# Performance work log

Measured on AMD Instinct MI355X. Metric: run time of the kernel, lower is better.

## Reference

```python
import jax, jax.numpy as jnp
import numpy as np

B, S, D = 4, 1024, 1024
NH, DH = 16, 64
DI = 4096
EPS = 1e-5


def layer_norm(x, g, b):
    mu = jnp.mean(x, axis=-1, keepdims=True)
    var = jnp.mean(jnp.square(x - mu), axis=-1, keepdims=True)
    return (x - mu) * jax.lax.rsqrt(var + EPS) * g + b


def rel_shift(x):
    # x: [B, n, q, r] -> Transformer-XL relative shift + lower-tri mask
    b, n, q, r = x.shape
    zp = jnp.zeros((b, n, q, 1), x.dtype)
    xp = jnp.concatenate([zp, x], axis=3).reshape(b, n, r + 1, q)
    x = xp[:, :, 1:, :].reshape(b, n, q, r)
    tril = jnp.tril(jnp.ones((q, r), x.dtype), r - q)
    return x * tril[None, None]


def setup_inputs() -> dict:
    key = jax.random.key(0)
    ks = jax.random.split(key, 16)
    sc = 0.02
    return {
        "w": jax.random.normal(ks[0], (B, S, D), jnp.float32),
        "r": jax.random.normal(ks[1], (B, S, D), jnp.float32),
        "w_bias": jax.random.normal(ks[2], (NH, 1, DH), jnp.float32) * sc,
        "r_bias": jax.random.normal(ks[3], (NH, 1, DH), jnp.float32) * sc,
        "Wq": jax.random.normal(ks[4], (D, NH * DH), jnp.float32) * sc,
        "Wk": jax.random.normal(ks[5], (D, NH * DH), jnp.float32) * sc,
        "Wv": jax.random.normal(ks[6], (D, NH * DH), jnp.float32) * sc,
        "Wr": jax.random.normal(ks[7], (D, NH * DH), jnp.float32) * sc,
        "Wo": jax.random.normal(ks[8], (NH * DH, D), jnp.float32) * sc,
        "ln1_g": jnp.ones((D,), jnp.float32),
        "ln1_b": jnp.zeros((D,), jnp.float32),
        "W1": jax.random.normal(ks[9], (D, DI), jnp.float32) * sc,
        "b1": jnp.zeros((DI,), jnp.float32),
        "W2": jax.random.normal(ks[10], (DI, D), jnp.float32) * sc,
        "b2": jnp.zeros((D,), jnp.float32),
        "ln2_g": jnp.ones((D,), jnp.float32),
        "ln2_b": jnp.zeros((D,), jnp.float32),
    }


def reference(w, r, w_bias, r_bias, Wq, Wk, Wv, Wr, Wo,
              ln1_g, ln1_b, W1, b1, W2, b2, ln2_g, ln2_b):
    b, q_len, _ = w.shape
    k_len = q_len
    scale = 1.0 / (DH ** 0.5)

    def heads(x):
        return x.reshape(b, -1, NH, DH).transpose(0, 2, 1, 3)  # [B, n, S, d]

    q = heads(w @ Wq)
    k = heads(w @ Wk)
    v = heads(w @ Wv)
    rr = heads(r @ Wr)

    ac = jnp.einsum('bnid,bnjd->bnij', q + w_bias[None], k)
    bd = rel_shift(jnp.einsum('bnid,bnjd->bnij', q + r_bias[None], rr))
    attn_score = (ac + bd) * scale

    mask = jnp.triu(jnp.ones((q_len, k_len), bool), 1)
    attn_score = jnp.where(mask[None, None], jnp.float32(-1e9), attn_score)
    attn_prob = jax.nn.softmax(attn_score, axis=-1)

    attn_vec = jnp.einsum('bnij,bnjd->bnid', attn_prob, v)
    attn_vec = attn_vec.transpose(0, 2, 1, 3).reshape(b, q_len, NH * DH)
    attn_out = attn_vec @ Wo

    x = layer_norm(w + attn_out, ln1_g, ln1_b)
    ff = jax.nn.relu(x @ W1 + b1) @ W2 + b2
    return layer_norm(x + ff, ln2_g, ln2_b)
```

## Files before the change

### kernel.cpp

```cpp
#include <hip/hip_runtime.h>
#include <hip/hip_bf16.h>

using bf16 = __hip_bfloat16;
typedef __attribute__((ext_vector_type(8))) short bf16x8;
typedef __attribute__((ext_vector_type(4))) float f32x4;

static constexpr int TB  = 4;
static constexpr int TS  = 1024;
static constexpr int TD  = 1024;
static constexpr int TNH = 16;
static constexpr int TDH = 64;
static constexpr int TDI = 4096;

__device__ __forceinline__ void gll16(const bf16* g, bf16* l)
{
    __builtin_amdgcn_global_load_lds(
        (const __attribute__((address_space(1))) void*)g,
        (__attribute__((address_space(3))) void*)l, 16, 0, 0);
}

__global__ __launch_bounds__(256) void zero_out_k(float* __restrict__ out, long n)
{
    long i = (long)blockIdx.x * 256 + threadIdx.x;
    if (i < n) out[i] = 0.0f;
}

__global__ __launch_bounds__(256) void convert2_f2b(const float* __restrict__ a,
                                                    const float* __restrict__ b,
                                                    bf16* __restrict__ oa,
                                                    bf16* __restrict__ ob, long n)
{
    const float* src = blockIdx.y ? b : a;
    bf16* dst = blockIdx.y ? ob : oa;
    long i = ((long)blockIdx.x * 256 + threadIdx.x) * 8;
    if (i >= n) return;
    float4 f0 = *(const float4*)(src + i);
    float4 f1 = *(const float4*)(src + i + 4);
    bf16 t[8] = {__float2bfloat16(f0.x), __float2bfloat16(f0.y),
                 __float2bfloat16(f0.z), __float2bfloat16(f0.w),
                 __float2bfloat16(f1.x), __float2bfloat16(f1.y),
                 __float2bfloat16(f1.z), __float2bfloat16(f1.w)};
    *(bf16x8*)(dst + i) = *(bf16x8*)t;
}

__global__ __launch_bounds__(256) void transpose_f2b(const float* __restrict__ in,
                                                     bf16* __restrict__ out,
                                                     int R, int C)
{
    __shared__ float tile[32][33];
    int c0 = blockIdx.x * 32, r0 = blockIdx.y * 32;
    int tx = threadIdx.x & 31, ty = threadIdx.x >> 5;
#pragma unroll
    for (int dy = 0; dy < 32; dy += 8)
        tile[ty + dy][tx] = in[(long)(r0 + ty + dy) * C + (c0 + tx)];
    __syncthreads();
#pragma unroll
    for (int dy = 0; dy < 32; dy += 8)
        out[(long)(c0 + ty + dy) * R + (r0 + tx)] = __float2bfloat16(tile[tx][ty + dy]);
}

__global__ __launch_bounds__(256) void transpose5_f2b(const float* __restrict__ p0,
                                                      const float* __restrict__ p1,
                                                      const float* __restrict__ p2,
                                                      const float* __restrict__ p3,
                                                      const float* __restrict__ p4,
                                                      bf16* __restrict__ dstBase)
{
    __shared__ float tile[32][33];
    const int D = TD;
    int z = blockIdx.z;
    const float* in = (z == 0) ? p0 : (z == 1) ? p1 : (z == 2) ? p2 : (z == 3) ? p3 : p4;
    bf16* out = dstBase + (long)z * D * D;
    int c0 = blockIdx.x * 32, r0 = blockIdx.y * 32;
    int tx = threadIdx.x & 31, ty = threadIdx.x >> 5;
#pragma unroll
    for (int dy = 0; dy < 32; dy += 8)
        tile[ty + dy][tx] = in[(long)(r0 + ty + dy) * D + (c0 + tx)];
    __syncthreads();
#pragma unroll
    for (int dy = 0; dy < 32; dy += 8)
        out[(long)(c0 + ty + dy) * D + (r0 + tx)] = __float2bfloat16(tile[tx][ty + dy]);
}

__global__ __launch_bounds__(256) void transpose_v(const bf16* __restrict__ V,
                                                   bf16* __restrict__ Vpk)
{
    __shared__ bf16 tile[32][33];
    int bn = blockIdx.z;
    int b = bn >> 4, n = bn & 15;
    const bf16* src = V + ((long)b * TS) * (TNH * TDH) + n * TDH;
    bf16* dst = Vpk + (long)bn * 65536;
    int s0 = blockIdx.x * 32, d0 = blockIdx.y * 32;
    int tx = threadIdx.x & 31, ty = threadIdx.x >> 5;
#pragma unroll
    for (int dy = 0; dy < 32; dy += 8)
        tile[ty + dy][tx] = src[(long)(s0 + ty + dy) * (TNH * TDH) + (d0 + tx)];
    __syncthreads();
#pragma unroll
    for (int dy = 0; dy < 32; dy += 8) {
        int d = d0 + ty + dy, s = s0 + tx;
        dst[((d >> 4) * 128 + (s >> 3)) * 128 + (d & 15) * 8 + (s & 7)] =
            tile[tx][ty + dy];
    }
}


__device__ __forceinline__ void stage_half(const bf16* __restrict__ X, long ldx,
                                           long rbase, long kcol,
                                           bf16* lds, int srow)
{
    gll16(X + (rbase + srow) * ldx + kcol, lds);
    gll16(X + (rbase + 128 + srow) * ldx + kcol, lds + 4096);
}

template<int MODE>
__global__ __launch_bounds__(512, 2) void gemm256_k(
    const bf16* __restrict__ A, long lda,
    const bf16* __restrict__ Bt, long ldb,
    bf16* __restrict__ O0, bf16* __restrict__ O1,
    bf16* __restrict__ O2, bf16* __restrict__ O3,
    float* __restrict__ F0, float* __restrict__ F1,
    float* __restrict__ F2, float* __restrict__ F3,
    const float* __restrict__ bias,
    int Kz, int GY, long ldc)
{
    __shared__ bf16 LDSbf[65536];

    const int z = blockIdx.y;
    const long kb = (long)z * Kz;
    const int NT = Kz >> 6;
    const int NI = NT >> 1;

    const int nwg = gridDim.x;
    const int orig = blockIdx.x;
    const int q = nwg >> 3, r = nwg & 7;
    const int xcd = orig & 7, idx = orig >> 3;
    const int wgid = (xcd < r ? xcd * (q + 1) : r * (q + 1) + (xcd - r) * q) + idx;

    int tx, ty;
    if (MODE == 1) {
        if (wgid < 192) { ty = wgid & 15; tx = wgid >> 4; }
        else { int w2 = wgid - 192; ty = 16 + (w2 & 15); tx = 12 + (w2 >> 4); }
    } else {
        ty = wgid % GY; tx = wgid / GY;
    }
    const long row0 = (long)ty * 256;
    const int col0 = tx * 256;

    const int tid = threadIdx.x;
    const int lane = tid & 63;
    const int wave = tid >> 6;
    const int wm2 = wave >> 2;
    const int wn4 = wave & 3;
    const int l15 = lane & 15;
    const int lq  = lane >> 4;

    const int slot = ((l15 & 1) << 2) | (lq ^ ((l15 >> 1) & 3));
    const int rdA = (wm2 * 64 + (l15 >> 1)) * 64 + slot * 8;
    const int rdB = 16384 + (wn4 * 32 + (l15 >> 1)) * 64 + slot * 8;

    const int srow  = wave * 16 + ((lane >> 3) << 1) + ((lane >> 2) & 1);
    const int scol8 = ((lane & 3) ^ ((lane >> 3) & 3)) * 8;

    f32x4 acc[8][4] = {};
    bf16x8 af[8], bb[4];

#define SA(t, db, kh) stage_half(A, lda, row0, kb + (long)(t) * 64 + (kh) * 32 + scol8, \
                                 LDSbf + (db) * 32768 + (kh) * 8192 + wave * 512, srow)
#define SB(t, db, kh) stage_half(Bt, ldb, (long)col0, kb + (long)(t) * 64 + (kh) * 32 + scol8, \
                                 LDSbf + (db) * 32768 + 16384 + (kh) * 8192 + wave * 512, srow)
#define RD_A(bp, kh) do {                                                              \
    _Pragma("unroll")                                                                  \
    for (int i_ = 0; i_ < 8; ++i_)                                                     \
        af[i_] = *(const bf16x8*)(LDSbf + (bp) * 32768 + (kh) * 8192 + rdA + i_ * 512);\
    } while (0)
#define RD_B(bp, kh, jh) do {                                                          \
    bb[(jh)*2]   = *(const bf16x8*)(LDSbf + (bp)*32768 + (kh)*8192 + rdB + ((jh)*2)*512);   \
    bb[(jh)*2+1] = *(const bf16x8*)(LDSbf + (bp)*32768 + (kh)*8192 + rdB + ((jh)*2+1)*512); \
    } while (0)
#define MM(jh) do {                                                                    \
    __builtin_amdgcn_s_setprio(1);                                                     \
    _Pragma("unroll")                                                                  \
    for (int i_ = 0; i_ < 8; ++i_) {                                                   \
        acc[i_][(jh)*2]   = __builtin_amdgcn_mfma_f32_16x16x32_bf16(af[i_], bb[(jh)*2],   acc[i_][(jh)*2],   0, 0, 0); \
        acc[i_][(jh)*2+1] = __builtin_amdgcn_mfma_f32_16x16x32_bf16(af[i_], bb[(jh)*2+1], acc[i_][(jh)*2+1], 0, 0, 0); \
    }                                                                                  \
    __builtin_amdgcn_s_setprio(0);                                                     \
    } while (0)
#define BAR       __builtin_amdgcn_s_barrier()
#define WLGKM0    do { asm volatile("s_waitcnt lgkmcnt(0)" ::: "memory");              \
                       __builtin_amdgcn_sched_barrier(0); } while (0)
#define WVM6      asm volatile("s_waitcnt vmcnt(6)" ::: "memory")

    SA(0, 0, 0); SB(0, 0, 0); SA(0, 0, 1); SB(0, 0, 1); SA(1, 1, 0);
    WVM6; BAR;

    for (int it = 0; it < NI; ++it) {
        const int T  = 2 * it;
        const int t1 = T + 1;
        const int t2 = (T + 2 < NT) ? T + 2 : NT - 1;
        const int t3 = (T + 3 < NT) ? T + 3 : NT - 1;

        RD_A(0, 0); RD_B(0, 0, 0); SB(t1, 1, 0);
        BAR; WLGKM0; MM(0); BAR;
        RD_B(0, 0, 1); SA(t1, 1, 1);
        BAR; WLGKM0; MM(1); WVM6; BAR;
        RD_A(0, 1); RD_B(0, 1, 0); SB(t1, 1, 1);
        BAR; WLGKM0; MM(0); BAR;
        RD_B(0, 1, 1); SA(t2, 0, 0);
        BAR; WLGKM0; MM(1); WVM6; BAR;
        RD_A(1, 0); RD_B(1, 0, 0); SB(t2, 0, 0);
        BAR; WLGKM0; MM(0); BAR;
        RD_B(1, 0, 1); SA(t2, 0, 1);
        BAR; WLGKM0; MM(1); WVM6; BAR;
        RD_A(1, 1); RD_B(1, 1, 0); SB(t2, 0, 1);
        BAR; WLGKM0; MM(0); BAR;
        RD_B(1, 1, 1); SA(t3, 1, 0);
        BAR; WLGKM0; MM(1); WVM6; BAR;
    }
    asm volatile("s_waitcnt vmcnt(0)" ::: "memory");

#undef SA
#undef SB
#undef RD_A
#undef RD_B
#undef MM
#undef BAR
#undef WLGKM0
#undef WVM6

    if (MODE == 0) {
        float* F = (z == 0) ? F0 : (z == 1) ? F1 : (z == 2) ? F2 : F3;
#pragma unroll
        for (int i = 0; i < 8; ++i) {
            long rb = (row0 + wm2 * 128 + i * 16 + lq * 4) * ldc;
#pragma unroll
            for (int j = 0; j < 4; ++j) {
                int nc = col0 + wn4 * 64 + j * 16 + l15;
#pragma unroll
                for (int rg = 0; rg < 4; ++rg)
                    F[rb + (long)rg * ldc + nc] = acc[i][j][rg];
            }
        }
    } else if (MODE == 1) {
        const int sel = tx >> 2;
        bf16* O = (sel == 0) ? O0 : (sel == 1) ? O1 : (sel == 2) ? O2 : O3;
        const int coladj = sel << 10;
        const long rowadj = (sel == 3) ? 4096 : 0;
#pragma unroll
        for (int i = 0; i < 8; ++i) {
            long mrow0 = row0 - rowadj + wm2 * 128 + i * 16 + lq * 4;
#pragma unroll
            for (int j = 0; j < 4; ++j) {
                int nc = col0 - coladj + wn4 * 64 + j * 16 + l15;
#pragma unroll
                for (int rg = 0; rg < 4; ++rg) {
                    float v = acc[i][j][rg];
                    if (sel == 0) v += bias[nc];
                    long mrow = mrow0 + rg;
                    if (sel == 2) {
                        O[mrow * 1024 + nc] = __float2bfloat16(v);
                    } else {
                        long b_ = mrow >> 10;
                        int s  = (int)mrow & 1023;
                        int n_ = nc >> 6, d = nc & 63;
                        long pidx = ((b_ * 16 + n_) << 16)
                                  + ((s >> 4) * 8 + (d >> 3)) * 128
                                  + (s & 15) * 8 + (d & 7);
                        O[pidx] = __float2bfloat16(v);
                    }
                }
            }
        }
    } else {
#pragma unroll
        for (int i = 0; i < 8; ++i) {
            long rb = (row0 + wm2 * 128 + i * 16 + lq * 4) * ldc;
#pragma unroll
            for (int j = 0; j < 4; ++j) {
                int nc = col0 + wn4 * 64 + j * 16 + l15;
#pragma unroll
                for (int rg = 0; rg < 4; ++rg) {
                    float v = acc[i][j][rg] + bias[nc];
                    v = fmaxf(v, 0.0f);
                    O0[rb + (long)rg * ldc + nc] = __float2bfloat16(v);
                }
            }
        }
    }
}

__global__ __launch_bounds__(64, 2) void flash_attn(
    const bf16* __restrict__ Qpk, const bf16* __restrict__ Kpk,
    const bf16* __restrict__ RRpk, const bf16* __restrict__ Vpk,
    const float* __restrict__ wbias, const float* __restrict__ rbias,
    bf16* __restrict__ Oa)
{
    const int S = TS, D = TD;
    __shared__ bf16 scr[32 * 161];

    const int orig = blockIdx.x;
    const int xcd = orig & 7, idx = orig >> 3;
    const int bn = xcd * 8 + (idx & 7);
    const int rem = idx >> 3;
    const int it = 7 - (rem >> 2);
    const int dw = (rem & 3) * 32;
    const int i0 = it * 128;
    const int b = bn >> 4, n = bn & 15;

    const int lane = threadIdx.x;
    const int l15 = lane & 15, lq = lane >> 4;

    const bf16* Qb = Qpk  + (long)bn * 65536;
    const bf16* Kb = Kpk  + (long)bn * 65536;
    const bf16* Rb = RRpk + (long)bn * 65536;
    const bf16* Vb = Vpk  + (long)bn * 65536;

    bf16x8 afw[2][2], afr[2][2];
#pragma unroll
    for (int m = 0; m < 2; ++m)
#pragma unroll
        for (int ks = 0; ks < 2; ++ks) {
            afw[m][ks] = *(const bf16x8*)(
                Qb + ((((i0 + dw) >> 4) + m) * 8 + ks * 4 + lq) * 128 + l15 * 8);
            bf16 tmp[8];
#pragma unroll
            for (int jj = 0; jj < 8; ++jj) {
                int di_ = n * 64 + ks * 32 + lq * 8 + jj;
                float f = __bfloat162float(((const bf16*)&afw[m][ks])[jj])
                          + rbias[di_] - wbias[di_];
                tmp[jj] = __float2bfloat16(f);
            }
            afr[m][ks] = *(bf16x8*)tmp;
        }

    float mst[2][4], lst[2][4];
    f32x4 Oacc[2][4] = {};
#pragma unroll
    for (int m = 0; m < 2; ++m)
#pragma unroll
        for (int rg = 0; rg < 4; ++rg) { mst[m][rg] = -1e30f; lst[m][rg] = 0.0f; }

    const int cofsg = 992 - i0 - dw;

    for (int jt = 0; jt <= it; ++jt) {
        const int j0 = jt * 128;
        const int rbt = (j0 + cofsg) >> 4;

#pragma unroll
        for (int g = 0; g < 2; ++g) {
            f32x4 bdl[2][5] = {};
#pragma unroll
            for (int ks = 0; ks < 2; ++ks) {
                bf16x8 bfr[5];
#pragma unroll
                for (int f = 0; f < 5; ++f) {
                    int t = rbt + g * 5 + f;
                    if (t > 63) t = 63;
                    bfr[f] = *(const bf16x8*)(Rb + (t * 8 + ks * 4 + lq) * 128 + l15 * 8);
                }
#pragma unroll
                for (int m = 0; m < 2; ++m)
#pragma unroll
                    for (int f = 0; f < 5; ++f)
                        bdl[m][f] = __builtin_amdgcn_mfma_f32_16x16x32_bf16(
                            afr[m][ks], bfr[f], bdl[m][f], 0, 0, 0);
            }
#pragma unroll
            for (int m = 0; m < 2; ++m)
#pragma unroll
                for (int f = 0; f < 5; ++f)
#pragma unroll
                    for (int rg = 0; rg < 4; ++rg) {
                        int ldi = lq * 4 + rg + 16 * m;
                        scr[ldi * 161 + (g * 5 + f) * 16 + l15] =
                            __float2bfloat16(bdl[m][f][rg]);
                    }
        }

        f32x4 ac[2][8] = {};
#pragma unroll
        for (int ks = 0; ks < 2; ++ks) {
            bf16x8 bk[8];
#pragma unroll
            for (int f = 0; f < 8; ++f)
                bk[f] = *(const bf16x8*)(
                    Kb + (((j0 >> 4) + f) * 8 + ks * 4 + lq) * 128 + l15 * 8);
#pragma unroll
            for (int m = 0; m < 2; ++m)
#pragma unroll
                for (int f = 0; f < 8; ++f)
                    ac[m][f] = __builtin_amdgcn_mfma_f32_16x16x32_bf16(
                        afw[m][ks], bk[f], ac[m][f], 0, 0, 0);
        }

        const bool diag = (jt == it);
#pragma unroll
        for (int m = 0; m < 2; ++m)
#pragma unroll
            for (int nf = 0; nf < 8; ++nf)
#pragma unroll
                for (int rg = 0; rg < 4; ++rg) {
                    int ldi = lq * 4 + rg + 16 * m;
                    int col = nf * 16 + l15;
                    float bdv = __bfloat162float(scr[ldi * 161 + (col + 31 - ldi)]);
                    float s = (ac[m][nf][rg] + bdv) * 0.125f;
                    if (diag && (col > dw + ldi)) s = -1e30f;
                    ac[m][nf][rg] = s;
                }

        float alpha[2][4];
#pragma unroll
        for (int m = 0; m < 2; ++m)
#pragma unroll
            for (int rg = 0; rg < 4; ++rg) {
                float v = -1e30f;
#pragma unroll
                for (int nf = 0; nf < 8; ++nf) v = fmaxf(v, ac[m][nf][rg]);
                for (int o = 8; o; o >>= 1) v = fmaxf(v, __shfl_xor(v, o));
                float mn = fmaxf(mst[m][rg], v);
                alpha[m][rg] = __expf(mst[m][rg] - mn);
                mst[m][rg] = mn;
            }
#pragma unroll
        for (int m = 0; m < 2; ++m)
#pragma unroll
            for (int nf = 0; nf < 8; ++nf)
#pragma unroll
                for (int rg = 0; rg < 4; ++rg)
                    ac[m][nf][rg] = __expf(ac[m][nf][rg] - mst[m][rg]);
#pragma unroll
        for (int m = 0; m < 2; ++m)
#pragma unroll
            for (int rg = 0; rg < 4; ++rg) {
                float sv = 0.0f;
#pragma unroll
                for (int nf = 0; nf < 8; ++nf) sv += ac[m][nf][rg];
                for (int o = 8; o; o >>= 1) sv += __shfl_xor(sv, o);
                lst[m][rg] = lst[m][rg] * alpha[m][rg] + sv;
            }
#pragma unroll
        for (int m = 0; m < 2; ++m)
#pragma unroll
            for (int nf = 0; nf < 4; ++nf)
#pragma unroll
                for (int rg = 0; rg < 4; ++rg)
                    Oacc[m][nf][rg] *= alpha[m][rg];

#pragma unroll
        for (int m = 0; m < 2; ++m)
#pragma unroll
            for (int nf = 0; nf < 8; ++nf)
#pragma unroll
                for (int rg = 0; rg < 4; ++rg) {
                    int ldi = lq * 4 + rg + 16 * m;
                    scr[ldi * 136 + nf * 16 + l15] = __float2bfloat16(ac[m][nf][rg]);
                }
#pragma unroll
        for (int ks2 = 0; ks2 < 4; ++ks2) {
            bf16x8 pa[2];
#pragma unroll
            for (int m = 0; m < 2; ++m)
                pa[m] = *(const bf16x8*)(&scr[(16 * m + l15) * 136 + ks2 * 32 + lq * 8]);
            bf16x8 vb[4];
#pragma unroll
            for (int nf = 0; nf < 4; ++nf)
                vb[nf] = *(const bf16x8*)(
                    Vb + (nf * 128 + (j0 >> 3) + ks2 * 4 + lq) * 128 + l15 * 8);
#pragma unroll
            for (int m = 0; m < 2; ++m)
#pragma unroll
                for (int nf = 0; nf < 4; ++nf)
                    Oacc[m][nf] = __builtin_amdgcn_mfma_f32_16x16x32_bf16(
                        pa[m], vb[nf], Oacc[m][nf], 0, 0, 0);
        }
    }

#pragma unroll
    for (int m = 0; m < 2; ++m)
#pragma unroll
        for (int rg = 0; rg < 4; ++rg) {
            float inv = 1.0f / lst[m][rg];
#pragma unroll
            for (int nf = 0; nf < 4; ++nf) {
                int row = i0 + dw + lq * 4 + rg + 16 * m;
                int col = nf * 16 + l15;
                Oa[((long)(b * S + row)) * D + n * 64 + col] =
                    __float2bfloat16(Oacc[m][nf][rg] * inv);
            }
        }
}

__global__ __launch_bounds__(256) void layernorm_f(const float* __restrict__ A0,
                                                   const float* __restrict__ A1,
                                                   const float* __restrict__ A2,
                                                   const float* __restrict__ A3,
                                                   const float* __restrict__ bias,
                                                   const float* __restrict__ residf,
                                                   const bf16* __restrict__ residb,
                                                   const float* __restrict__ g,
                                                   const float* __restrict__ beta,
                                                   float* __restrict__ Yf,
                                                   bf16* __restrict__ Yb)
{
    const int D = TD;
    long row = blockIdx.x;
    int tid = threadIdx.x;
    int wave = tid >> 6;

    float v[4], s = 0.0f;
#pragma unroll
    for (int it = 0; it < 4; ++it) {
        int c = tid + it * 256;
        float x = A0[row * D + c] + A1[row * D + c] + A2[row * D + c] + A3[row * D + c];
        if (bias)   x += bias[c];
        if (residf) x += residf[row * D + c];
        if (residb) x += __bfloat162float(residb[row * D + c]);
        v[it] = x; s += x;
    }
    for (int off = 32; off; off >>= 1) s += __shfl_xor(s, off);
    __shared__ float sm[8];
    if ((tid & 63) == 0) sm[wave] = s;
    __syncthreads();
    float mean = (sm[0] + sm[1] + sm[2] + sm[3]) * (1.0f / D);

    float var = 0.0f;
#pragma unroll
    for (int it = 0; it < 4; ++it) { float d = v[it] - mean; var += d * d; }
    for (int off = 32; off; off >>= 1) var += __shfl_xor(var, off);
    if ((tid & 63) == 0) sm[4 + wave] = var;
    __syncthreads();
    var = (sm[4] + sm[5] + sm[6] + sm[7]) * (1.0f / D);
    float rinv = rsqrtf(var + 1e-5f);

#pragma unroll
    for (int it = 0; it < 4; ++it) {
        int c = tid + it * 256;
        float o = (v[it] - mean) * rinv * g[c] + beta[c];
        if (Yf) Yf[row * D + c] = o;
        if (Yb) Yb[row * D + c] = __float2bfloat16(o);
    }
}

extern "C" void kernel_launch(void* const* d_in, const int* in_sizes, int n_in,
                              void* d_out, int out_size, void* d_ws, size_t ws_size,
                              hipStream_t stream)
{
    const float* w      = (const float*)d_in[0];
    const float* r      = (const float*)d_in[1];
    const float* w_bias = (const float*)d_in[2];
    const float* r_bias = (const float*)d_in[3];
    const float* Wq     = (const float*)d_in[4];
    const float* Wk     = (const float*)d_in[5];
    const float* Wv     = (const float*)d_in[6];
    const float* Wr     = (const float*)d_in[7];
    const float* Wo     = (const float*)d_in[8];
    const float* ln1_g  = (const float*)d_in[9];
    const float* ln1_b  = (const float*)d_in[10];
    const float* W1     = (const float*)d_in[11];
    const float* b1     = (const float*)d_in[12];
    const float* W2     = (const float*)d_in[13];
    const float* b2     = (const float*)d_in[14];
    const float* ln2_g  = (const float*)d_in[15];
    const float* ln2_b  = (const float*)d_in[16];
    float* out = (float*)d_out;

    const int  B = TB, S = TS, D = TD, NH = TNH, DH = TDH, DI = TDI;
    const long MS = (long)B * S;
    const long ND = (long)MS * D;

    char* base = (char*)d_ws;
    size_t off = 0;
    auto alloc = [&](size_t bytes) -> void* {
        void* p = base + off;
        off += (bytes + 255) & ~(size_t)255;
        return p;
    };
    bf16* wqT  = (bf16*)alloc(2UL * D * D);
    bf16* wkT  = (bf16*)alloc(2UL * D * D);
    bf16* wvT  = (bf16*)alloc(2UL * D * D);
    bf16* wrT  = (bf16*)alloc(2UL * D * D);
    bf16* woT  = (bf16*)alloc(2UL * D * D);
    bf16* w1T  = (bf16*)alloc(2UL * D * DI);
    bf16* w2T  = (bf16*)alloc(2UL * DI * D);
    bf16* bufA = (bf16*)alloc(2UL * ND);
    bf16* bufB = (bf16*)alloc(2UL * ND);
    bf16* Qpk  = (bf16*)alloc(2UL * ND);
    bf16* Kpk  = (bf16*)alloc(2UL * ND);
    bf16* RRpk = (bf16*)alloc(2UL * ND);
    bf16* Vpk  = (bf16*)alloc(2UL * ND);
    bf16* R0   = (bf16*)alloc(2UL * MS * DI);
    size_t need = off;
    (void)in_sizes; (void)n_in; (void)out_size;

    if (ws_size < need) {
        zero_out_k<<<dim3((unsigned)((ND + 255) / 256)), 256, 0, stream>>>(out, ND);
        return;
    }

    bf16* w_bf = bufA;  bf16* attn_vec = bufA;
    bf16* r_bf = bufB;  bf16* x_bf     = bufB;
    bf16* Vb   = R0;    bf16* h        = R0;
    float* Pf  = (float*)Qpk;

    convert2_f2b<<<dim3((unsigned)(ND / (8 * 256)), 2), 256, 0, stream>>>(
        w, r, w_bf, r_bf, ND);
    transpose5_f2b<<<dim3(D / 32, D / 32, 5), 256, 0, stream>>>(
        Wq, Wk, Wv, Wr, Wo, wqT);
    transpose_f2b<<<dim3(DI / 32, D / 32), 256, 0, stream>>>(W1, w1T, D, DI);
    transpose_f2b<<<dim3(D / 32, DI / 32), 256, 0, stream>>>(W2, w2T, DI, D);

    gemm256_k<1><<<dim3(256, 1), 512, 0, stream>>>(
        w_bf, D, wqT, D, Qpk, Kpk, Vb, RRpk,
        nullptr, nullptr, nullptr, nullptr, w_bias, D, 16, D);
    transpose_v<<<dim3(S / 32, DH / 32, B * NH), 256, 0, stream>>>(Vb, Vpk);

    flash_attn<<<dim3(2048), 64, 0, stream>>>(Qpk, Kpk, RRpk, Vpk, w_bias, r_bias,
                                              attn_vec);

    gemm256_k<0><<<dim3(64, 4), 512, 0, stream>>>(
        attn_vec, D, woT, D, nullptr, nullptr, nullptr, nullptr,
        Pf, Pf + ND, Pf + 2 * ND, Pf + 3 * ND, nullptr, D / 4, 16, D);
    layernorm_f<<<dim3((unsigned)MS), 256, 0, stream>>>(
        Pf, Pf + ND, Pf + 2 * ND, Pf + 3 * ND, nullptr, w, nullptr,
        ln1_g, ln1_b, nullptr, x_bf);

    gemm256_k<2><<<dim3(256, 1), 512, 0, stream>>>(
        x_bf, D, w1T, D, h, nullptr, nullptr, nullptr,
        nullptr, nullptr, nullptr, nullptr, b1, D, 16, DI);

    gemm256_k<0><<<dim3(64, 4), 512, 0, stream>>>(
        h, DI, w2T, DI, nullptr, nullptr, nullptr, nullptr,
        Pf, Pf + ND, (float*)wqT, out, nullptr, DI / 4, 16, D);
    layernorm_f<<<dim3((unsigned)MS), 256, 0, stream>>>(
        Pf, Pf + ND, (float*)wqT, out, b2, nullptr, x_bf,
        ln2_g, ln2_b, out, nullptr);
}
```

Baseline: 411.1 us.

## Replace split-K output GEMMs with 128-tile GEMMs, fuse V packing, shrink attention tiles

The Wo and W2 projections no longer use a 4-way split-K 256-tile GEMM that wrote four fp32 partials for layernorm to sum. They now use a new 128x128-tile GEMM that adds bias and residual in its epilogue and writes a single fp32 result, which a simpler layernorm reads. The QKV GEMM writes V directly in the packed layout the attention kernel needs, so the separate transpose kernel is removed. Flash attention processes 16 query rows per wave instead of 32, with twice as many blocks and higher occupancy, at the cost of more K/V reloads across waves.

```diff
diff --git a/kernel.cpp b/kernel.cpp
--- a/kernel.cpp
+++ b/kernel.cpp
@@ -82,28 +82,6 @@
         out[(long)(c0 + ty + dy) * D + (r0 + tx)] = __float2bfloat16(tile[tx][ty + dy]);
 }
 
-__global__ __launch_bounds__(256) void transpose_v(const bf16* __restrict__ V,
-                                                   bf16* __restrict__ Vpk)
-{
-    __shared__ bf16 tile[32][33];
-    int bn = blockIdx.z;
-    int b = bn >> 4, n = bn & 15;
-    const bf16* src = V + ((long)b * TS) * (TNH * TDH) + n * TDH;
-    bf16* dst = Vpk + (long)bn * 65536;
-    int s0 = blockIdx.x * 32, d0 = blockIdx.y * 32;
-    int tx = threadIdx.x & 31, ty = threadIdx.x >> 5;
-#pragma unroll
-    for (int dy = 0; dy < 32; dy += 8)
-        tile[ty + dy][tx] = src[(long)(s0 + ty + dy) * (TNH * TDH) + (d0 + tx)];
-    __syncthreads();
-#pragma unroll
-    for (int dy = 0; dy < 32; dy += 8) {
-        int d = d0 + ty + dy, s = s0 + tx;
-        dst[((d >> 4) * 128 + (s >> 3)) * 128 + (d & 15) * 8 + (s & 7)] =
-            tile[tx][ty + dy];
-    }
-}
-
 
 __device__ __forceinline__ void stage_half(const bf16* __restrict__ X, long ldx,
                                            long rbase, long kcol,
@@ -119,16 +97,12 @@
     const bf16* __restrict__ Bt, long ldb,
     bf16* __restrict__ O0, bf16* __restrict__ O1,
     bf16* __restrict__ O2, bf16* __restrict__ O3,
-    float* __restrict__ F0, float* __restrict__ F1,
-    float* __restrict__ F2, float* __restrict__ F3,
     const float* __restrict__ bias,
-    int Kz, int GY, long ldc)
+    int K, int GY, long ldc)
 {
     __shared__ bf16 LDSbf[65536];
 
-    const int z = blockIdx.y;
-    const long kb = (long)z * Kz;
-    const int NT = Kz >> 6;
+    const int NT = K >> 6;
     const int NI = NT >> 1;
 
     const int nwg = gridDim.x;
@@ -165,9 +139,9 @@
     f32x4 acc[8][4] = {};
     bf16x8 af[8], bb[4];
 
-#define SA(t, db, kh) stage_half(A, lda, row0, kb + (long)(t) * 64 + (kh) * 32 + scol8, \
+#define SA(t, db, kh) stage_half(A, lda, row0, (long)(t) * 64 + (kh) * 32 + scol8, \
                                  LDSbf + (db) * 32768 + (kh) * 8192 + wave * 512, srow)
-#define SB(t, db, kh) stage_half(Bt, ldb, (long)col0, kb + (long)(t) * 64 + (kh) * 32 + scol8, \
+#define SB(t, db, kh) stage_half(Bt, ldb, (long)col0, (long)(t) * 64 + (kh) * 32 + scol8, \
                                  LDSbf + (db) * 32768 + 16384 + (kh) * 8192 + wave * 512, srow)
 #define RD_A(bp, kh) do {                                                              \
     _Pragma("unroll")                                                                  \
@@ -229,20 +203,7 @@
 #undef WLGKM0
 #undef WVM6
 
-    if (MODE == 0) {
-        float* F = (z == 0) ? F0 : (z == 1) ? F1 : (z == 2) ? F2 : F3;
-#pragma unroll
-        for (int i = 0; i < 8; ++i) {
-            long rb = (row0 + wm2 * 128 + i * 16 + lq * 4) * ldc;
-#pragma unroll
-            for (int j = 0; j < 4; ++j) {
-                int nc = col0 + wn4 * 64 + j * 16 + l15;
-#pragma unroll
-                for (int rg = 0; rg < 4; ++rg)
-                    F[rb + (long)rg * ldc + nc] = acc[i][j][rg];
-            }
-        }
-    } else if (MODE == 1) {
+    if (MODE == 1) {
         const int sel = tx >> 2;
         bf16* O = (sel == 0) ? O0 : (sel == 1) ? O1 : (sel == 2) ? O2 : O3;
         const int coladj = sel << 10;
@@ -258,17 +219,18 @@
                     float v = acc[i][j][rg];
                     if (sel == 0) v += bias[nc];
                     long mrow = mrow0 + rg;
+                    long b_ = mrow >> 10;
+                    int s  = (int)mrow & 1023;
+                    int n_ = nc >> 6, d = nc & 63;
+                    long pidx;
                     if (sel == 2) {
-                        O[mrow * 1024 + nc] = __float2bfloat16(v);
+                        pidx = ((b_ * 16 + n_) << 16)
+                             + ((d >> 4) * 128 + (s >> 3)) * 128 + (d & 15) * 8 + (s & 7);
                     } else {
-                        long b_ = mrow >> 10;
-                        int s  = (int)mrow & 1023;
-                        int n_ = nc >> 6, d = nc & 63;
-                        long pidx = ((b_ * 16 + n_) << 16)
-                                  + ((s >> 4) * 8 + (d >> 3)) * 128
-                                  + (s & 15) * 8 + (d & 7);
-                        O[pidx] = __float2bfloat16(v);
+                        pidx = ((b_ * 16 + n_) << 16)
+                             + ((s >> 4) * 8 + (d >> 3)) * 128 + (s & 15) * 8 + (d & 7);
                     }
+                    O[pidx] = __float2bfloat16(v);
                 }
             }
         }
@@ -290,22 +252,137 @@
     }
 }
 
-__global__ __launch_bounds__(64, 2) void flash_attn(
+template<int MODE>
+__global__ __launch_bounds__(512, 2) void gemm128_k(
+    const bf16* __restrict__ A, long lda,
+    const bf16* __restrict__ Bt, long ldb,
+    float* __restrict__ Zf,
+    const float* __restrict__ residf, const bf16* __restrict__ residb,
+    const float* __restrict__ bias,
+    int K, int GY, long ldc)
+{
+    __shared__ bf16 LDSbf[32768];
+
+    const int NT = K >> 6;
+    const int NI = NT >> 1;
+
+    const int nwg = gridDim.x;
+    const int orig = blockIdx.x;
+    const int q = nwg >> 3, r = nwg & 7;
+    const int xcd = orig & 7, idx = orig >> 3;
+    const int wgid = (xcd < r ? xcd * (q + 1) : r * (q + 1) + (xcd - r) * q) + idx;
+
+    const int ty = wgid % GY, tx = wgid / GY;
+    const long row0 = (long)ty * 128;
+    const long col0 = (long)tx * 128;
+
+    const int tid = threadIdx.x;
+    const int lane = tid & 63;
+    const int wave = tid >> 6;
+    const int wm2 = wave >> 2;
+    const int wn4 = wave & 3;
+    const int l15 = lane & 15;
+    const int lq  = lane >> 4;
+
+    const int slot = ((l15 & 1) << 2) | (lq ^ ((l15 >> 1) & 3));
+    const int rdA = (wm2 * 32 + (l15 >> 1)) * 64 + slot * 8;
+    const int rdB = 8192 + (wn4 * 16 + (l15 >> 1)) * 64 + slot * 8;
+
+    const int srow  = (tid >> 3) * 2 + ((tid >> 2) & 1);
+    const int scol8 = ((tid & 3) ^ ((tid >> 3) & 3)) * 8;
+
+    f32x4 acc[4][2] = {};
+    bf16x8 af[4], bb[2];
+
+#define SA(t, db, kh) gll16(A + (row0 + srow) * lda + (long)(t) * 64 + (kh) * 32 + scol8, \
+                            LDSbf + (db) * 16384 + (kh) * 4096 + wave * 512)
+#define SB(t, db, kh) gll16(Bt + (col0 + srow) * ldb + (long)(t) * 64 + (kh) * 32 + scol8, \
+                            LDSbf + (db) * 16384 + 8192 + (kh) * 4096 + wave * 512)
+#define RD(db, kh) do {                                                                \
+    _Pragma("unroll")                                                                  \
+    for (int i_ = 0; i_ < 4; ++i_)                                                     \
+        af[i_] = *(const bf16x8*)(LDSbf + (db) * 16384 + (kh) * 4096 + rdA + i_ * 512);\
+    _Pragma("unroll")                                                                  \
+    for (int j_ = 0; j_ < 2; ++j_)                                                     \
+        bb[j_] = *(const bf16x8*)(LDSbf + (db) * 16384 + (kh) * 4096 + rdB + j_ * 512);\
+    } while (0)
+#define MM8 do {                                                                       \
+    __builtin_amdgcn_s_setprio(1);                                                     \
+    _Pragma("unroll")                                                                  \
+    for (int i_ = 0; i_ < 4; ++i_) {                                                   \
+        acc[i_][0] = __builtin_amdgcn_mfma_f32_16x16x32_bf16(af[i_], bb[0], acc[i_][0], 0, 0, 0); \
+        acc[i_][1] = __builtin_amdgcn_mfma_f32_16x16x32_bf16(af[i_], bb[1], acc[i_][1], 0, 0, 0); \
+    }                                                                                  \
+    __builtin_amdgcn_s_setprio(0);                                                     \
+    } while (0)
+#define BAR       __builtin_amdgcn_s_barrier()
+#define WLGKM0    do { asm volatile("s_waitcnt lgkmcnt(0)" ::: "memory");              \
+                       __builtin_amdgcn_sched_barrier(0); } while (0)
+#define WVM4      asm volatile("s_waitcnt vmcnt(4)" ::: "memory")
+
+    SA(0, 0, 0); SB(0, 0, 0); SA(0, 0, 1); SB(0, 0, 1); SA(1, 1, 0); SB(1, 1, 0);
+    WVM4; BAR;
+
+    for (int it = 0; it < NI; ++it) {
+        const int T  = 2 * it;
+        const int t1 = T + 1;
+        const int t2 = (T + 2 < NT) ? T + 2 : NT - 1;
+        const int t3 = (T + 3 < NT) ? T + 3 : NT - 1;
+
+        RD(0, 0); SA(t1, 1, 1); SB(t1, 1, 1);
+        BAR; WLGKM0; MM8; WVM4; BAR;
+        RD(0, 1); SA(t2, 0, 0); SB(t2, 0, 0);
+        BAR; WLGKM0; MM8; WVM4; BAR;
+        RD(1, 0); SA(t2, 0, 1); SB(t2, 0, 1);
+        BAR; WLGKM0; MM8; WVM4; BAR;
+        RD(1, 1); SA(t3, 1, 0); SB(t3, 1, 0);
+        BAR; WLGKM0; MM8; WVM4; BAR;
+    }
+    asm volatile("s_waitcnt vmcnt(0)" ::: "memory");
+
+#undef SA
+#undef SB
+#undef RD
+#undef MM8
+#undef BAR
+#undef WLGKM0
+#undef WVM4
+
+#pragma unroll
+    for (int i = 0; i < 4; ++i) {
+        long mrow0 = row0 + wm2 * 64 + i * 16 + lq * 4;
+#pragma unroll
+        for (int j = 0; j < 2; ++j) {
+            int nc = (int)col0 + wn4 * 32 + j * 16 + l15;
+#pragma unroll
+            for (int rg = 0; rg < 4; ++rg) {
+                long ridx = (mrow0 + rg) * ldc + nc;
+                float v = acc[i][j][rg];
+                if (MODE == 3) v += residf[ridx];
+                else           v += bias[nc] + __bfloat162float(residb[ridx]);
+                Zf[ridx] = v;
+            }
+        }
+    }
+}
+
+__global__ __launch_bounds__(64, 4) void flash_attn(
     const bf16* __restrict__ Qpk, const bf16* __restrict__ Kpk,
     const bf16* __restrict__ RRpk, const bf16* __restrict__ Vpk,
     const float* __restrict__ wbias, const float* __restrict__ rbias,
     bf16* __restrict__ Oa)
 {
     const int S = TS, D = TD;
-    __shared__ bf16 scr[32 * 161];
+    __shared__ bf16 scr[16 * 161];
 
     const int orig = blockIdx.x;
     const int xcd = orig & 7, idx = orig >> 3;
     const int bn = xcd * 8 + (idx & 7);
     const int rem = idx >> 3;
-    const int it = 7 - (rem >> 2);
-    const int dw = (rem & 3) * 32;
-    const int i0 = it * 128;
+    const int r16 = 63 - rem;
+    const int it = r16 >> 3;
+    const int rowstart = r16 * 16;
+    const int dwq = (r16 & 7) * 16;
     const int b = bn >> 4, n = bn & 15;
 
     const int lane = threadIdx.x;
@@ -316,69 +393,65 @@
     const bf16* Rb = RRpk + (long)bn * 65536;
     const bf16* Vb = Vpk  + (long)bn * 65536;
 
-    bf16x8 afw[2][2], afr[2][2];
-#pragma unroll
-    for (int m = 0; m < 2; ++m)
-#pragma unroll
-        for (int ks = 0; ks < 2; ++ks) {
-            afw[m][ks] = *(const bf16x8*)(
-                Qb + ((((i0 + dw) >> 4) + m) * 8 + ks * 4 + lq) * 128 + l15 * 8);
-            bf16 tmp[8];
-#pragma unroll
-            for (int jj = 0; jj < 8; ++jj) {
-                int di_ = n * 64 + ks * 32 + lq * 8 + jj;
-                float f = __bfloat162float(((const bf16*)&afw[m][ks])[jj])
-                          + rbias[di_] - wbias[di_];
-                tmp[jj] = __float2bfloat16(f);
-            }
-            afr[m][ks] = *(bf16x8*)tmp;
-        }
-
-    float mst[2][4], lst[2][4];
-    f32x4 Oacc[2][4] = {};
-#pragma unroll
-    for (int m = 0; m < 2; ++m)
-#pragma unroll
-        for (int rg = 0; rg < 4; ++rg) { mst[m][rg] = -1e30f; lst[m][rg] = 0.0f; }
-
-    const int cofsg = 992 - i0 - dw;
+    bf16x8 afw[2], afr[2];
+#pragma unroll
+    for (int ks = 0; ks < 2; ++ks) {
+        afw[ks] = *(const bf16x8*)(Qb + (r16 * 8 + ks * 4 + lq) * 128 + l15 * 8);
+        bf16 tmp[8];
+#pragma unroll
+        for (int jj = 0; jj < 8; ++jj) {
+            int di_ = n * 64 + ks * 32 + lq * 8 + jj;
+            float f = __bfloat162float(((const bf16*)&afw[ks])[jj])
+                      + rbias[di_] - wbias[di_];
+            tmp[jj] = __float2bfloat16(f);
+        }
+        afr[ks] = *(bf16x8*)tmp;
+    }
+
+    float mst[4], lst[4];
+    f32x4 Oacc[4] = {};
+#pragma unroll
+    for (int rg = 0; rg < 4; ++rg) { mst[rg] = -1e30f; lst[rg] = 0.0f; }
+
+    const int cofs16 = 1008 - rowstart;
 
     for (int jt = 0; jt <= it; ++jt) {
         const int j0 = jt * 128;
-        const int rbt = (j0 + cofsg) >> 4;
+        const int rbt = (j0 + cofs16) >> 4;
 
 #pragma unroll
         for (int g = 0; g < 2; ++g) {
-            f32x4 bdl[2][5] = {};
+            const int NF = g ? 4 : 5;
+            f32x4 bdl[5] = {};
 #pragma unroll
             for (int ks = 0; ks < 2; ++ks) {
                 bf16x8 bfr[5];
 #pragma unroll
                 for (int f = 0; f < 5; ++f) {
-                    int t = rbt + g * 5 + f;
-                    if (t > 63) t = 63;
-                    bfr[f] = *(const bf16x8*)(Rb + (t * 8 + ks * 4 + lq) * 128 + l15 * 8);
+                    if (f < NF) {
+                        int t = rbt + g * 5 + f;
+                        if (t > 63) t = 63;
+                        bfr[f] = *(const bf16x8*)(Rb + (t * 8 + ks * 4 + lq) * 128 + l15 * 8);
+                    }
                 }
 #pragma unroll
-                for (int m = 0; m < 2; ++m)
-#pragma unroll
-                    for (int f = 0; f < 5; ++f)
-                        bdl[m][f] = __builtin_amdgcn_mfma_f32_16x16x32_bf16(
-                            afr[m][ks], bfr[f], bdl[m][f], 0, 0, 0);
+                for (int f = 0; f < 5; ++f)
+                    if (f < NF)
+                        bdl[f] = __builtin_amdgcn_mfma_f32_16x16x32_bf16(
+                            afr[ks], bfr[f], bdl[f], 0, 0, 0);
             }
 #pragma unroll
-            for (int m = 0; m < 2; ++m)
-#pragma unroll
-                for (int f = 0; f < 5; ++f)
+            for (int f = 0; f < 5; ++f)
+                if (f < NF)
 #pragma unroll
                     for (int rg = 0; rg < 4; ++rg) {
-                        int ldi = lq * 4 + rg + 16 * m;
+                        int ldi = lq * 4 + rg;
                         scr[ldi * 161 + (g * 5 + f) * 16 + l15] =
-                            __float2bfloat16(bdl[m][f][rg]);
+                            __float2bfloat16(bdl[f][rg]);
                     }
         }
 
-        f32x4 ac[2][8] = {};
+        f32x4 ac[8] = {};
 #pragma unroll
         for (int ks = 0; ks < 2; ++ks) {
             bf16x8 bk[8];
@@ -387,121 +460,94 @@
                 bk[f] = *(const bf16x8*)(
                     Kb + (((j0 >> 4) + f) * 8 + ks * 4 + lq) * 128 + l15 * 8);
 #pragma unroll
-            for (int m = 0; m < 2; ++m)
-#pragma unroll
-                for (int f = 0; f < 8; ++f)
-                    ac[m][f] = __builtin_amdgcn_mfma_f32_16x16x32_bf16(
-                        afw[m][ks], bk[f], ac[m][f], 0, 0, 0);
+            for (int f = 0; f < 8; ++f)
+                ac[f] = __builtin_amdgcn_mfma_f32_16x16x32_bf16(
+                    afw[ks], bk[f], ac[f], 0, 0, 0);
         }
 
         const bool diag = (jt == it);
 #pragma unroll
-        for (int m = 0; m < 2; ++m)
-#pragma unroll
-            for (int nf = 0; nf < 8; ++nf)
-#pragma unroll
-                for (int rg = 0; rg < 4; ++rg) {
-                    int ldi = lq * 4 + rg + 16 * m;
-                    int col = nf * 16 + l15;
-                    float bdv = __bfloat162float(scr[ldi * 161 + (col + 31 - ldi)]);
-                    float s = (ac[m][nf][rg] + bdv) * 0.125f;
-                    if (diag && (col > dw + ldi)) s = -1e30f;
-                    ac[m][nf][rg] = s;
-                }
-
-        float alpha[2][4];
-#pragma unroll
-        for (int m = 0; m < 2; ++m)
+        for (int nf = 0; nf < 8; ++nf)
 #pragma unroll
             for (int rg = 0; rg < 4; ++rg) {
-                float v = -1e30f;
-#pragma unroll
-                for (int nf = 0; nf < 8; ++nf) v = fmaxf(v, ac[m][nf][rg]);
-                for (int o = 8; o; o >>= 1) v = fmaxf(v, __shfl_xor(v, o));
-                float mn = fmaxf(mst[m][rg], v);
-                alpha[m][rg] = __expf(mst[m][rg] - mn);
-                mst[m][rg] = mn;
+                int ldi = lq * 4 + rg;
+                int col = nf * 16 + l15;
+                float bdv = __bfloat162float(scr[ldi * 161 + (col + 15 - ldi)]);
+                float s = (ac[nf][rg] + bdv) * 0.125f;
+                if (diag && (col > dwq + ldi)) s = -1e30f;
+                ac[nf][rg] = s;
             }
-#pragma unroll
-        for (int m = 0; m < 2; ++m)
-#pragma unroll
-            for (int nf = 0; nf < 8; ++nf)
-#pragma unroll
-                for (int rg = 0; rg < 4; ++rg)
-                    ac[m][nf][rg] = __expf(ac[m][nf][rg] - mst[m][rg]);
-#pragma unroll
-        for (int m = 0; m < 2; ++m)
+
+        float alpha[4];
+#pragma unroll
+        for (int rg = 0; rg < 4; ++rg) {
+            float v = -1e30f;
+#pragma unroll
+            for (int nf = 0; nf < 8; ++nf) v = fmaxf(v, ac[nf][rg]);
+            for (int o = 8; o; o >>= 1) v = fmaxf(v, __shfl_xor(v, o));
+            float mn = fmaxf(mst[rg], v);
+            alpha[rg] = __expf(mst[rg] - mn);
+            mst[rg] = mn;
+        }
+#pragma unroll
+        for (int nf = 0; nf < 8; ++nf)
+#pragma unroll
+            for (int rg = 0; rg < 4; ++rg)
+                ac[nf][rg] = __expf(ac[nf][rg] - mst[rg]);
+#pragma unroll
+        for (int rg = 0; rg < 4; ++rg) {
+            float sv = 0.0f;
+#pragma unroll
+            for (int nf = 0; nf < 8; ++nf) sv += ac[nf][rg];
+            for (int o = 8; o; o >>= 1) sv += __shfl_xor(sv, o);
+            lst[rg] = lst[rg] * alpha[rg] + sv;
+        }
+#pragma unroll
+        for (int nf = 0; nf < 4; ++nf)
+#pragma unroll
+            for (int rg = 0; rg < 4; ++rg)
+                Oacc[nf][rg] *= alpha[rg];
+
+#pragma unroll
+        for (int nf = 0; nf < 8; ++nf)
 #pragma unroll
             for (int rg = 0; rg < 4; ++rg) {
-                float sv = 0.0f;
-#pragma unroll
-                for (int nf = 0; nf < 8; ++nf) sv += ac[m][nf][rg];
-                for (int o = 8; o; o >>= 1) sv += __shfl_xor(sv, o);
-                lst[m][rg] = lst[m][rg] * alpha[m][rg] + sv;
+                int ldi = lq * 4 + rg;
+                scr[ldi * 136 + nf * 16 + l15] = __float2bfloat16(ac[nf][rg]);
             }
 #pragma unroll
-        for (int m = 0; m < 2; ++m)
-#pragma unroll
-            for (int nf = 0; nf < 4; ++nf)
-#pragma unroll
-                for (int rg = 0; rg < 4; ++rg)
-                    Oacc[m][nf][rg] *= alpha[m][rg];
-
-#pragma unroll
-        for (int m = 0; m < 2; ++m)
-#pragma unroll
-            for (int nf = 0; nf < 8; ++nf)
-#pragma unroll
-                for (int rg = 0; rg < 4; ++rg) {
-                    int ldi = lq * 4 + rg + 16 * m;
-                    scr[ldi * 136 + nf * 16 + l15] = __float2bfloat16(ac[m][nf][rg]);
-                }
-#pragma unroll
         for (int ks2 = 0; ks2 < 4; ++ks2) {
-            bf16x8 pa[2];
-#pragma unroll
-            for (int m = 0; m < 2; ++m)
-                pa[m] = *(const bf16x8*)(&scr[(16 * m + l15) * 136 + ks2 * 32 + lq * 8]);
+            bf16x8 pa = *(const bf16x8*)(&scr[l15 * 136 + ks2 * 32 + lq * 8]);
             bf16x8 vb[4];
 #pragma unroll
             for (int nf = 0; nf < 4; ++nf)
                 vb[nf] = *(const bf16x8*)(
                     Vb + (nf * 128 + (j0 >> 3) + ks2 * 4 + lq) * 128 + l15 * 8);
 #pragma unroll
-            for (int m = 0; m < 2; ++m)
-#pragma unroll
-                for (int nf = 0; nf < 4; ++nf)
-                    Oacc[m][nf] = __builtin_amdgcn_mfma_f32_16x16x32_bf16(
-                        pa[m], vb[nf], Oacc[m][nf], 0, 0, 0);
-        }
-    }
-
-#pragma unroll
-    for (int m = 0; m < 2; ++m)
-#pragma unroll
-        for (int rg = 0; rg < 4; ++rg) {
-            float inv = 1.0f / lst[m][rg];
-#pragma unroll
-            for (int nf = 0; nf < 4; ++nf) {
-                int row = i0 + dw + lq * 4 + rg + 16 * m;
-                int col = nf * 16 + l15;
-                Oa[((long)(b * S + row)) * D + n * 64 + col] =
-                    __float2bfloat16(Oacc[m][nf][rg] * inv);
-            }
-        }
-}
-
-__global__ __launch_bounds__(256) void layernorm_f(const float* __restrict__ A0,
-                                                   const float* __restrict__ A1,
-                                                   const float* __restrict__ A2,
-                                                   const float* __restrict__ A3,
-                                                   const float* __restrict__ bias,
-                                                   const float* __restrict__ residf,
-                                                   const bf16* __restrict__ residb,
-                                                   const float* __restrict__ g,
-                                                   const float* __restrict__ beta,
-                                                   float* __restrict__ Yf,
-                                                   bf16* __restrict__ Yb)
+            for (int nf = 0; nf < 4; ++nf)
+                Oacc[nf] = __builtin_amdgcn_mfma_f32_16x16x32_bf16(
+                    pa, vb[nf], Oacc[nf], 0, 0, 0);
+        }
+    }
+
+#pragma unroll
+    for (int rg = 0; rg < 4; ++rg) {
+        float inv = 1.0f / lst[rg];
+#pragma unroll
+        for (int nf = 0; nf < 4; ++nf) {
+            int row = rowstart + lq * 4 + rg;
+            int col = nf * 16 + l15;
+            Oa[((long)(b * S + row)) * D + n * 64 + col] =
+                __float2bfloat16(Oacc[nf][rg] * inv);
+        }
+    }
+}
+
+__global__ __launch_bounds__(256) void ln_single(const float* __restrict__ Zf,
+                                                 const float* __restrict__ g,
+                                                 const float* __restrict__ beta,
+                                                 float* __restrict__ Yf,
+                                                 bf16* __restrict__ Yb)
 {
     const int D = TD;
     long row = blockIdx.x;
@@ -512,10 +558,7 @@
 #pragma unroll
     for (int it = 0; it < 4; ++it) {
         int c = tid + it * 256;
-        float x = A0[row * D + c] + A1[row * D + c] + A2[row * D + c] + A3[row * D + c];
-        if (bias)   x += bias[c];
-        if (residf) x += residf[row * D + c];
-        if (residb) x += __bfloat162float(residb[row * D + c]);
+        float x = Zf[row * D + c];
         v[it] = x; s += x;
     }
     for (int off = 32; off; off >>= 1) s += __shfl_xor(s, off);
@@ -600,7 +643,7 @@
 
     bf16* w_bf = bufA;  bf16* attn_vec = bufA;
     bf16* r_bf = bufB;  bf16* x_bf     = bufB;
-    bf16* Vb   = R0;    bf16* h        = R0;
+    bf16* h    = R0;
     float* Pf  = (float*)Qpk;
 
     convert2_f2b<<<dim3((unsigned)(ND / (8 * 256)), 2), 256, 0, stream>>>(
@@ -611,28 +654,19 @@
     transpose_f2b<<<dim3(D / 32, DI / 32), 256, 0, stream>>>(W2, w2T, DI, D);
 
     gemm256_k<1><<<dim3(256, 1), 512, 0, stream>>>(
-        w_bf, D, wqT, D, Qpk, Kpk, Vb, RRpk,
-        nullptr, nullptr, nullptr, nullptr, w_bias, D, 16, D);
-    transpose_v<<<dim3(S / 32, DH / 32, B * NH), 256, 0, stream>>>(Vb, Vpk);
-
-    flash_attn<<<dim3(2048), 64, 0, stream>>>(Qpk, Kpk, RRpk, Vpk, w_bias, r_bias,
+        w_bf, D, wqT, D, Qpk, Kpk, Vpk, RRpk, w_bias, D, 16, D);
+
+    flash_attn<<<dim3(4096), 64, 0, stream>>>(Qpk, Kpk, RRpk, Vpk, w_bias, r_bias,
                                               attn_vec);
 
-    gemm256_k<0><<<dim3(64, 4), 512, 0, stream>>>(
-        attn_vec, D, woT, D, nullptr, nullptr, nullptr, nullptr,
-        Pf, Pf + ND, Pf + 2 * ND, Pf + 3 * ND, nullptr, D / 4, 16, D);
-    layernorm_f<<<dim3((unsigned)MS), 256, 0, stream>>>(
-        Pf, Pf + ND, Pf + 2 * ND, Pf + 3 * ND, nullptr, w, nullptr,
-        ln1_g, ln1_b, nullptr, x_bf);
+    gemm128_k<3><<<dim3(256, 1), 512, 0, stream>>>(
+        attn_vec, D, woT, D, Pf, w, nullptr, nullptr, D, 32, D);
+    ln_single<<<dim3((unsigned)MS), 256, 0, stream>>>(Pf, ln1_g, ln1_b, nullptr, x_bf);
 
     gemm256_k<2><<<dim3(256, 1), 512, 0, stream>>>(
-        x_bf, D, w1T, D, h, nullptr, nullptr, nullptr,
-        nullptr, nullptr, nullptr, nullptr, b1, D, 16, DI);
-
-    gemm256_k<0><<<dim3(64, 4), 512, 0, stream>>>(
-        h, DI, w2T, DI, nullptr, nullptr, nullptr, nullptr,
-        Pf, Pf + ND, (float*)wqT, out, nullptr, DI / 4, 16, D);
-    layernorm_f<<<dim3((unsigned)MS), 256, 0, stream>>>(
-        Pf, Pf + ND, (float*)wqT, out, b2, nullptr, x_bf,
-        ln2_g, ln2_b, out, nullptr);
-}
+        x_bf, D, w1T, D, h, nullptr, nullptr, nullptr, b1, D, 16, DI);
+
+    gemm128_k<4><<<dim3(256, 1), 512, 0, stream>>>(
+        h, DI, w2T, DI, Pf, nullptr, x_bf, b2, DI, 32, D);
+    ln_single<<<dim3((unsigned)MS), 256, 0, stream>>>(Pf, ln2_g, ln2_b, out, nullptr);
+}
```

Result: faster. 370.6 us (-9.9%).
